# Kernel optimization log

Measured on AMD Instinct MI355X. Metric: run time of the kernel, lower is better.

The kernel has to match this reference:

```python
import jax, jax.numpy as jnp
import numpy as np

B, N, H, FD = 2, 512, 128, 5
NT, SD, L = 3, 4, 3
COPY = 10.0
EPS = 1e-6


def setup_inputs() -> dict:
    key = jax.random.key(0)
    ks = jax.random.split(key, 20)
    node_type = jax.random.randint(ks[0], (B, N, 1), 0, NT).astype(jnp.float32)
    node_state = jax.random.normal(ks[1], (B, N, SD), jnp.float32)
    node_feats = jnp.concatenate([node_type, node_state], axis=-1)  # [B,N,5]
    adj = jax.random.bernoulli(ks[2], 0.05, (B, N, N)).astype(jnp.float32)
    adj = jnp.maximum(adj, adj.transpose(0, 2, 1)) * (1.0 - jnp.eye(N, dtype=jnp.float32))
    scope_node_mask = jax.random.bernoulli(ks[3], 0.5, (B, N)).astype(jnp.float32)
    scope_edge_mask = jax.random.bernoulli(ks[4], 0.5, (B, N, N)).astype(jnp.float32)
    s = 0.02
    p = dict(
        node_feats=node_feats, adj=adj,
        scope_node_mask=scope_node_mask, scope_edge_mask=scope_edge_mask,
        W_in=jax.random.normal(ks[5], (FD, H)) * s, b_in=jnp.zeros((H,)),
        W_mp=jax.random.normal(ks[6], (L, 2 * H, H)) * s, b_mp=jnp.zeros((L, H)),
        Wt1=jax.random.normal(ks[7], (H, H)) * s, bt1=jnp.zeros((H,)),
        Wt2=jax.random.normal(ks[8], (H, NT)) * s, bt2=jnp.zeros((NT,)),
        Ws1=jax.random.normal(ks[9], (H, H)) * s, bs1=jnp.zeros((H,)),
        Ws2=jax.random.normal(ks[10], (H, SD)) * s, bs2=jnp.zeros((SD,)),
        We1=jax.random.normal(ks[11], (4 * H, H)) * s, be1=jnp.zeros((H,)),
        We2=jax.random.normal(ks[12], (H, 3)) * s, be2=jnp.zeros((3,)),
    )
    return p


def _decode_edge_logits(adj, edl, eye):
    probs = jax.nn.softmax(edl, axis=-1)
    p_keep = probs[..., 0]  # EDGE_DELTA_KEEP = 0
    p_add = probs[..., 1]   # EDGE_DELTA_ADD = 1
    cur = (adj > 0.5).astype(edl.dtype)
    p_next = jnp.clip(p_add + p_keep * cur, EPS, 1.0 - EPS)
    el = jnp.log(p_next) - jnp.log1p(-p_next)  # logit
    return jnp.where(eye[None], -1e9, el)


def _forward(node_feats, adj, scope_node_mask, scope_edge_mask,
             W_in, b_in, W_mp, b_mp, Wt1, bt1, Wt2, bt2,
             Ws1, bs1, Ws2, bs2, We1, be1, We2, be2):
    # encoder: input proj + L rounds of [h, adj@h] -> Linear -> ReLU
    h = jax.nn.relu(node_feats @ W_in + b_in)  # [B,N,H]
    for l in range(L):
        msg = jnp.einsum('bij,bjh->bih', adj, h)
        h = jax.nn.relu(jnp.concatenate([h, msg], axis=-1) @ W_mp[l] + b_mp[l])
    # node heads (2-layer MLPs)
    type_local = jax.nn.relu(h @ Wt1 + bt1) @ Wt2 + bt2      # [B,N,NT]
    state_local = jax.nn.relu(h @ Ws1 + bs1) @ Ws2 + bs2     # [B,N,SD]
    # pairwise edge-delta head
    h_i = h[:, :, None, :]
    h_j = h[:, None, :, :]
    pair = jnp.concatenate([
        jnp.broadcast_to(h_i, (B, N, N, H)),
        jnp.broadcast_to(h_j, (B, N, N, H)),
        jnp.abs(h_i - h_j),
        h_i * h_j,
    ], axis=-1)  # [B,N,N,4H]
    edl = jax.nn.relu(pair @ We1 + be1) @ We2 + be2  # [B,N,N,3]
    edl = 0.5 * (edl + edl.transpose(0, 2, 1, 3))
    eye = jnp.eye(N, dtype=bool)
    edl = jnp.where(eye[None, :, :, None], 0.0, edl)
    # merges with copy paths
    cur_type = jnp.clip(node_feats[..., 0].astype(jnp.int32), 0, NT - 1)
    copy_type = jnp.where(jnp.arange(NT) == cur_type[..., None], COPY, -COPY)
    type_full = jnp.where(scope_node_mask[..., None] != 0, type_local, copy_type)
    scope = scope_node_mask[..., None]
    state_full = scope * state_local + (1.0 - scope) * node_feats[..., 1:]
    copy_edl = jnp.broadcast_to(jnp.where(jnp.arange(3) == 0, COPY, -COPY), (B, N, N, 3))
    copy_edl = jnp.where(eye[None, :, :, None], 0.0, copy_edl)
    edl_full = jnp.where(scope_edge_mask[..., None] != 0, edl, copy_edl)
    el_full = _decode_edge_logits(adj, edl_full, eye)
    return type_full, state_full, edl_full, el_full


def reference(node_feats, adj, scope_node_mask, scope_edge_mask,
              W_in, b_in, W_mp, b_mp, Wt1, bt1, Wt2, bt2,
              Ws1, bs1, Ws2, bs2, We1, be1, We2, be2):
    return _forward(node_feats, adj, scope_node_mask, scope_edge_mask,
                    W_in, b_in, W_mp, b_mp, Wt1, bt1, Wt2, bt2,
                    Ws1, bs1, Ws2, bs2, We1, be1, We2, be2)
```

## Files before the change

### kernel.cpp

```cpp
#include <hip/hip_runtime.h>
#include <hip/hip_fp16.h>
#include <math.h>

#define B_ 2
#define N_ 512
#define H_ 128
#define NT_ 3
#define SD_ 4
#define FD_ 5

typedef float f32x4 __attribute__((ext_vector_type(4)));
typedef unsigned int u32x4 __attribute__((ext_vector_type(4)));

#define MFMA4(a0, a1, a2, a3, av, b0, b1, b2, b3) \
    asm("s_nop 1\n\t" \
        "v_mfma_f32_16x16x32_f16 %0, %4, %5, %0\n\t" \
        "v_mfma_f32_16x16x32_f16 %1, %4, %6, %1\n\t" \
        "v_mfma_f32_16x16x32_f16 %2, %4, %7, %2\n\t" \
        "v_mfma_f32_16x16x32_f16 %3, %4, %8, %3" \
        : "+v"(a0), "+v"(a1), "+v"(a2), "+v"(a3) \
        : "v"(av), "v"(b0), "v"(b1), "v"(b2), "v"(b3))

#define MFMA16F(acc, a, b) \
    asm("s_nop 1\n\tv_mfma_f32_16x16x32_f16 %0, %1, %2, %0" \
        : "+v"(acc) : "v"(a), "v"(b))

#define PKMUL(d, a, b) \
    asm("v_pk_mul_f16 %0, %1, %2" : "=v"(d) : "v"(a), "v"(b))
#define PKSUB(d, a, b) \
    asm("v_pk_add_f16 %0, %1, %2 neg_lo:[0,1] neg_hi:[0,1]" \
        : "=v"(d) : "v"(a), "v"(b))
#define CVTPKF16(d, a, b) \
    asm("v_cvt_pkrtz_f16_f32 %0, %1, %2" : "=v"(d) : "v"(a), "v"(b))

static __device__ inline unsigned short f2h(float f) {
    return __half_as_ushort(__float2half(f));
}

__global__ __launch_bounds__(128) void k_input(const float* __restrict__ feats,
                                               const float* __restrict__ W_in,
                                               const float* __restrict__ b_in,
                                               float* __restrict__ hout,
                                               const float* __restrict__ We1,
                                               const float* __restrict__ We2,
                                               unsigned short* __restrict__ wfrag,
                                               unsigned short* __restrict__ wfrag2) {
    int blk = blockIdx.x, tid = threadIdx.x;
    if (blk < B_ * N_) {
        const float* f = feats + (size_t)blk * FD_;
        float acc = b_in[tid];
#pragma unroll
        for (int k = 0; k < FD_; ++k) acc += f[k] * W_in[k * H_ + tid];
        hout[(size_t)blk * H_ + tid] = fmaxf(acc, 0.f);
        return;
    }
    if (blk < B_ * N_ + 32) {
        int t = (blk - B_ * N_) * 128 + tid;
        int lane = t & 63, cg = (t >> 6) & 7, kb = t >> 9;
        int lr = lane & 15, g = lane >> 4;
        int c = cg * 16 + lr;
        unsigned o[4];
#pragma unroll
        for (int p = 0; p < 4; ++p) {
            float a = We1[(size_t)(256 + kb * 32 + 8 * g + 2 * p) * H_ + c];
            float bq = We1[(size_t)(256 + kb * 32 + 8 * g + 2 * p + 1) * H_ + c];
            o[p] = (unsigned)f2h(a) | ((unsigned)f2h(bq) << 16);
        }
        u32x4 v = {o[0], o[1], o[2], o[3]};
        *(u32x4*)(wfrag + (size_t)t * 8) = v;
        return;
    }
    {
        int t = (blk - (B_ * N_ + 32)) * 128 + tid;
        if (t < 256) {
            int kb = t >> 6, lane = t & 63;
            int oc = lane & 15, g = lane >> 4;
            unsigned w[4];
#pragma unroll
            for (int p = 0; p < 4; ++p) {
                int k0 = kb * 32 + g * 8 + 2 * p;
                int k1 = k0 + 1;
                int c0 = ((k0 >> 6) << 6) | ((k0 & 3) << 4) | ((k0 & 63) >> 2);
                int c1 = ((k1 >> 6) << 6) | ((k1 & 3) << 4) | ((k1 & 63) >> 2);
                float v0 = (oc < 3) ? We2[c0 * 3 + oc] : 0.f;
                float v1 = (oc < 3) ? We2[c1 * 3 + oc] : 0.f;
                w[p] = (unsigned)f2h(v0) | ((unsigned)f2h(v1) << 16);
            }
            u32x4 v = {w[0], w[1], w[2], w[3]};
            *(u32x4*)(wfrag2 + (size_t)t * 8) = v;
        }
    }
}

__global__ __launch_bounds__(256) void k_mp(const float* __restrict__ hin,
                                            float* __restrict__ hout,
                                            const float* __restrict__ adj,
                                            const float* __restrict__ Wl,
                                            const float* __restrict__ bl) {
    __shared__ float xbuf[256];
    __shared__ unsigned short idxs[512];
    __shared__ float avals[512];
    __shared__ float red[256];
    __shared__ int cnt[4];
    int node = blockIdx.x;
    int b = node >> 9;
    int tid = threadIdx.x;
    int w = tid >> 6, lane = tid & 63;
    if (tid < 128) xbuf[tid] = hin[(size_t)node * H_ + tid];
    const float* arow = adj + (size_t)node * N_;
    float2 av = ((const float2*)arow)[tid];
    int cum = 0;
#pragma unroll
    for (int q2 = 0; q2 < 2; ++q2) {
        float a = (&av.x)[q2];
        bool pred = (a != 0.f);
        unsigned long long mask = __ballot(pred);
        if (pred) {
            int pos = 128 * w + cum +
                      (int)__popcll(mask & ((1ull << lane) - 1ull));
            idxs[pos] = (unsigned short)(2 * tid + q2);
            avals[pos] = a;
        }
        cum += (int)__popcll(mask);
    }
    if (lane == 0) cnt[w] = cum;
    __syncthreads();

    int c = tid & 127, q = tid >> 7;
    const float* hb = hin + ((size_t)b * N_) * H_;
    float m = 0.f;
#pragma unroll
    for (int s = 0; s < 4; ++s) {
        int ns = cnt[s];
        for (int t = q; t < ns; t += 2)
            m += avals[128 * s + t] * hb[(size_t)idxs[128 * s + t] * H_ + c];
    }
    red[q * 128 + c] = m;
    __syncthreads();
    if (q == 0) xbuf[128 + c] = red[c] + red[128 + c];
    __syncthreads();

    float acc = 0.f;
#pragma unroll 4
    for (int k = 128 * q; k < 128 * q + 128; ++k)
        acc += xbuf[k] * Wl[(size_t)k * H_ + c];
    red[q * 128 + c] = acc;
    __syncthreads();
    if (q == 0)
        hout[(size_t)node * H_ + c] =
            fmaxf(red[c] + red[128 + c] + bl[c], 0.f);
}

__global__ __launch_bounds__(128) void k_heads(
    const float* __restrict__ h, const float* __restrict__ feats,
    const float* __restrict__ snm,
    const float* __restrict__ Wt1, const float* __restrict__ bt1,
    const float* __restrict__ Wt2, const float* __restrict__ bt2,
    const float* __restrict__ Ws1, const float* __restrict__ bs1,
    const float* __restrict__ Ws2, const float* __restrict__ bs2,
    const float* __restrict__ We1, const float* __restrict__ be1,
    float* __restrict__ Acoef, float* __restrict__ Bcoef,
    unsigned short* __restrict__ hf16,
    float* __restrict__ type_out, float* __restrict__ state_out) {
    __shared__ float hi[H_], hT[H_], hS[H_];
    int node = blockIdx.x, tid = threadIdx.x;
    float hv0 = h[(size_t)node * H_ + tid];
    hi[tid] = hv0;
    hf16[(size_t)node * H_ + tid] = f2h(hv0);
    __syncthreads();
    float at = bt1[tid], as = bs1[tid], aa = be1[tid], ab = 0.f;
#pragma unroll 4
    for (int k = 0; k < H_; ++k) {
        float hv = hi[k];
        at += hv * Wt1[k * H_ + tid];
        as += hv * Ws1[k * H_ + tid];
        aa += hv * We1[k * H_ + tid];
        ab += hv * We1[(k + H_) * H_ + tid];
    }
    hT[tid] = fmaxf(at, 0.f);
    hS[tid] = fmaxf(as, 0.f);
    int c = tid;
    int kp = ((c >> 6) << 6) | ((c & 15) << 2) | ((c >> 4) & 3);
    Acoef[(size_t)node * H_ + kp] = aa;
    Bcoef[(size_t)node * H_ + kp] = ab;
    __syncthreads();
    float sm = snm[node];
    if (tid < NT_) {
        float tl = bt2[tid];
        for (int cc = 0; cc < H_; ++cc) tl += hT[cc] * Wt2[cc * NT_ + tid];
        int ct = (int)feats[(size_t)node * FD_];
        ct = ct < 0 ? 0 : (ct > NT_ - 1 ? NT_ - 1 : ct);
        float cv = (tid == ct) ? 10.f : -10.f;
        type_out[(size_t)node * NT_ + tid] = (sm != 0.f) ? tl : cv;
    }
    if (tid >= 64 && tid < 64 + SD_) {
        int s = tid - 64;
        float sl = bs2[s];
        for (int cc = 0; cc < H_; ++cc) sl += hS[cc] * Ws2[cc * SD_ + s];
        state_out[(size_t)node * SD_ + s] =
            sm * sl + (1.f - sm) * feats[(size_t)node * FD_ + 1 + s];
    }
}

__global__ __launch_bounds__(256, 2) void k_pair2(
    const unsigned short* __restrict__ hf16,
    const float* __restrict__ Acp, const float* __restrict__ Bcp,
    const unsigned short* __restrict__ wfrag,
    const unsigned short* __restrict__ wfrag2,
    const float* __restrict__ be2,
    float* __restrict__ edl_out) {

    __shared__ unsigned short tile[2][64][128];
    __shared__ float sbuf[2][64][3];

    int bid = blockIdx.x;
    int b = 0, r = bid;
    if (r >= 1280) { b = 1; r -= 1280; }
    int jtile, i;
    if (r < 128)      { jtile = 0; i = r; }
    else if (r < 384) { jtile = 1; i = r - 128; }
    else if (r < 768) { jtile = 2; i = r - 384; }
    else              { jtile = 3; i = r - 768; }
    int JT0 = jtile << 7;
    int bN = b << 9;

    int tid = threadIdx.x;
    int wave = tid >> 6, lane = tid & 63;
    int jh = wave >> 1, ch = wave & 1;
    int lr = lane & 15, g = lane >> 4;

    u32x4 Bf[4][8];
#pragma unroll
    for (int ct = 0; ct < 4; ++ct)
#pragma unroll
        for (int kb = 0; kb < 8; ++kb)
            Bf[ct][kb] = *(const u32x4*)(wfrag +
                (((size_t)kb * 8 + (ch * 4 + ct)) * 64 + lane) * 8);

    u32x4 Bf2[4];
#pragma unroll
    for (int kb = 0; kb < 4; ++kb)
        Bf2[kb] = *(const u32x4*)(wfrag2 + ((size_t)kb * 64 + lane) * 8);

    const unsigned short* hirow = hf16 + (size_t)(bN + i) * H_;
    u32x4 him[4];
#pragma unroll
    for (int m = 0; m < 4; ++m)
        him[m] = *(const u32x4*)(hirow + 32 * m + 8 * g);

    f32x4 AcoI = *(const f32x4*)(Acp + (size_t)(bN + i) * H_ + ch * 64 + lr * 4);
    f32x4 BcoI = *(const f32x4*)(Bcp + (size_t)(bN + i) * H_ + ch * 64 + lr * 4);

    char* tb0 = (char*)&tile[0][0][0];
    char* tb1 = (char*)&tile[1][0][0];

    for (int jhalf = 0; jhalf < 2; ++jhalf) {
        int J0 = JT0 + jhalf * 64;
#pragma unroll
        for (int jt = 0; jt < 2; ++jt) {
            int jloc0 = jh * 32 + jt * 16;
            const unsigned short* hjp =
                hf16 + (size_t)(bN + J0 + jloc0 + lr) * H_ + 8 * g;
            u32x4 hjall[4];
#pragma unroll
            for (int m = 0; m < 4; ++m)
                hjall[m] = *(const u32x4*)(hjp + 32 * m);
            f32x4 BcJv[4], AcJv[4];
#pragma unroll
            for (int rr = 0; rr < 4; ++rr) {
                size_t jn = (size_t)(bN + J0 + jloc0 + 4 * g + rr) * H_ +
                            ch * 64 + lr * 4;
                BcJv[rr] = *(const f32x4*)(Bcp + jn);
                AcJv[rr] = *(const f32x4*)(Acp + jn);
            }

            f32x4 acc0 = {0.f,0.f,0.f,0.f}, acc1 = {0.f,0.f,0.f,0.f};
            f32x4 acc2 = {0.f,0.f,0.f,0.f}, acc3 = {0.f,0.f,0.f,0.f};

#pragma unroll
            for (int m = 0; m < 4; ++m) {
                u32x4 tav, uav;
#pragma unroll
                for (int p = 0; p < 4; ++p) {
                    unsigned hip_ = him[m][p], hjp_ = hjall[m][p];
                    unsigned u_, d_;
                    PKMUL(u_, hip_, hjp_);
                    PKSUB(d_, hip_, hjp_);
                    uav[p] = u_;
                    tav[p] = d_ & 0x7fff7fffu;
                }
                MFMA4(acc0, acc1, acc2, acc3, tav,
                      Bf[0][m], Bf[1][m], Bf[2][m], Bf[3][m]);
                MFMA4(acc0, acc1, acc2, acc3, uav,
                      Bf[0][4 + m], Bf[1][4 + m], Bf[2][4 + m], Bf[3][4 + m]);
            }
            asm("s_nop 7\n\ts_nop 7\n\ts_nop 3"
                : "+v"(acc0), "+v"(acc1), "+v"(acc2), "+v"(acc3));

#pragma unroll
            for (int rr = 0; rr < 4; ++rr) {
                int jloc = jloc0 + 4 * g + rr;
                float h10 = fmaxf(acc0[rr] + AcoI[0] + BcJv[rr][0], 0.f);
                float h11 = fmaxf(acc1[rr] + AcoI[1] + BcJv[rr][1], 0.f);
                float h12 = fmaxf(acc2[rr] + AcoI[2] + BcJv[rr][2], 0.f);
                float h13 = fmaxf(acc3[rr] + AcoI[3] + BcJv[rr][3], 0.f);
                float h20 = fmaxf(acc0[rr] + AcJv[rr][0] + BcoI[0], 0.f);
                float h21 = fmaxf(acc1[rr] + AcJv[rr][1] + BcoI[1], 0.f);
                float h22 = fmaxf(acc2[rr] + AcJv[rr][2] + BcoI[2], 0.f);
                float h23 = fmaxf(acc3[rr] + AcJv[rr][3] + BcoI[3], 0.f);
                unsigned w10, w11, w20, w21;
                CVTPKF16(w10, h10, h11); CVTPKF16(w11, h12, h13);
                CVTPKF16(w20, h20, h21); CVTPKF16(w21, h22, h23);
                int byte = jloc * 256 + ch * 128 + lr * 8;
                byte ^= (jloc & 7) << 4;
                uint2 v1; v1.x = w10; v1.y = w11;
                uint2 v2; v2.x = w20; v2.y = w21;
                *(uint2*)(tb0 + byte) = v1;
                *(uint2*)(tb1 + byte) = v2;
            }
        }
        __syncthreads();

        f32x4 pacc0 = {0.f,0.f,0.f,0.f}, pacc1 = {0.f,0.f,0.f,0.f};
#pragma unroll
        for (int p = 0; p < 2; ++p) {
            int f = wave + 4 * p;
            int orient = f >> 2, sub = f & 3;
            char* tb = orient ? tb1 : tb0;
            int jloc = sub * 16 + lr;
#pragma unroll
            for (int kb = 0; kb < 4; ++kb) {
                int byte = jloc * 256 + kb * 64 + g * 16;
                byte ^= (jloc & 7) << 4;
                u32x4 a = *(const u32x4*)(tb + byte);
                if (p == 0) { MFMA16F(pacc0, a, Bf2[kb]); }
                else        { MFMA16F(pacc1, a, Bf2[kb]); }
            }
        }
        asm("s_nop 7\n\ts_nop 7\n\ts_nop 3" : "+v"(pacc0), "+v"(pacc1));

        if (lr < 3) {
#pragma unroll
            for (int p = 0; p < 2; ++p) {
                int f = wave + 4 * p;
                int orient = f >> 2, sub = f & 3;
                f32x4 pa = p ? pacc1 : pacc0;
#pragma unroll
                for (int rr = 0; rr < 4; ++rr) {
                    int jloc = sub * 16 + 4 * g + rr;
                    sbuf[orient][jloc][lr] = pa[rr];
                }
            }
        }
        __syncthreads();

        if (tid < 192) {
            int jloc = tid / 3, comp = tid - jloc * 3;
            float v = 0.5f * (sbuf[0][jloc][comp] + sbuf[1][jloc][comp]) +
                      be2[comp];
            edl_out[((size_t)(bN + i) * N_ + (J0 + jloc)) * 3 + comp] = v;
        }
    }
}

__global__ __launch_bounds__(256) void k_tr(float* __restrict__ edl,
                                            float* __restrict__ el,
                                            const float* __restrict__ sem,
                                            const float* __restrict__ adj) {
    __shared__ float ss[3][16][17];
    int tid = threadIdx.x;
    int r = tid >> 4, c = tid & 15;
    int bid = blockIdx.x;
    int b = 0, t = bid;
    if (t >= 528) { b = 1; t -= 528; }
    int J = (int)((sqrtf(8.f * (float)t + 1.f) - 1.f) * 0.5f);
    while ((J + 1) * (J + 2) / 2 <= t) ++J;
    while (J * (J + 1) / 2 > t) --J;
    int I = t - J * (J + 1) / 2;
    int i0 = I * 16, j0 = J * 16;
    int bN = b << 9;

    {
        const float* src = edl + ((size_t)(bN + i0 + r) * N_ + (j0 + c)) * 3;
        ss[0][r][c] = src[0];
        ss[1][r][c] = src[1];
        ss[2][r][c] = src[2];
    }
    __syncthreads();

    for (int pass = 0; pass < 2; ++pass) {
        if (pass == 1 && I == J) break;
        int gi, gj;
        float s0, s1, s2;
        if (I == J) {
            gi = i0 + r; gj = j0 + c;
            int lo = r <= c ? r : c, hi = r <= c ? c : r;
            s0 = ss[0][lo][hi]; s1 = ss[1][lo][hi]; s2 = ss[2][lo][hi];
        } else if (pass == 0) {
            gi = i0 + r; gj = j0 + c;
            s0 = ss[0][r][c]; s1 = ss[1][r][c]; s2 = ss[2][r][c];
        } else {
            gi = j0 + r; gj = i0 + c;
            s0 = ss[0][c][r]; s1 = ss[1][c][r]; s2 = ss[2][c][r];
        }
        size_t p = (size_t)(bN + gi) * N_ + gj;
        if (gi == gj) {
            edl[p * 3 + 0] = 0.f; edl[p * 3 + 1] = 0.f; edl[p * 3 + 2] = 0.f;
            el[p] = -1e9f;
        } else {
            float msk = sem[p];
            float e0 = (msk != 0.f) ? s0 : 10.f;
            float e1 = (msk != 0.f) ? s1 : -10.f;
            float e2 = (msk != 0.f) ? s2 : -10.f;
            edl[p * 3 + 0] = e0; edl[p * 3 + 1] = e1; edl[p * 3 + 2] = e2;
            float a = adj[p];
            float cur = (a > 0.5f) ? 1.f : 0.f;
            float mx = fmaxf(e0, fmaxf(e1, e2));
            float x0 = expf(e0 - mx), x1 = expf(e1 - mx), x2 = expf(e2 - mx);
            float inv = 1.f / (x0 + x1 + x2);
            float pn = x1 * inv + x0 * inv * cur;
            pn = fminf(fmaxf(pn, 1e-6f), 1.f - 1e-6f);
            el[p] = logf(pn) - log1pf(-pn);
        }
    }
}

extern "C" void kernel_launch(void* const* d_in, const int* in_sizes, int n_in,
                              void* d_out, int out_size, void* d_ws,
                              size_t ws_size, hipStream_t stream) {
    const float* feats = (const float*)d_in[0];
    const float* adj   = (const float*)d_in[1];
    const float* snm   = (const float*)d_in[2];
    const float* sem   = (const float*)d_in[3];
    const float* W_in  = (const float*)d_in[4];
    const float* b_in  = (const float*)d_in[5];
    const float* W_mp  = (const float*)d_in[6];
    const float* b_mp  = (const float*)d_in[7];
    const float* Wt1 = (const float*)d_in[8],  *bt1 = (const float*)d_in[9];
    const float* Wt2 = (const float*)d_in[10], *bt2 = (const float*)d_in[11];
    const float* Ws1 = (const float*)d_in[12], *bs1 = (const float*)d_in[13];
    const float* Ws2 = (const float*)d_in[14], *bs2 = (const float*)d_in[15];
    const float* We1 = (const float*)d_in[16], *be1 = (const float*)d_in[17];
    const float* We2 = (const float*)d_in[18], *be2 = (const float*)d_in[19];

    float* out = (float*)d_out;
    float* type_out  = out;
    float* state_out = out + 3072;
    float* edl_out   = out + 7168;
    float* el_out    = out + 7168 + 1572864;

    float* ws = (float*)d_ws;
    float* hA = ws;
    float* hB = ws + 131072;
    float* Bcp = ws + 262144;
    unsigned short* hf16   = (unsigned short*)(ws + 393216);
    unsigned short* wfrag  = (unsigned short*)(ws + 458752);
    unsigned short* wfrag2 = (unsigned short*)(ws + 475136);
    float* Acp = hA;

    k_input<<<B_ * N_ + 34, 128, 0, stream>>>(feats, W_in, b_in, hA,
                                              We1, We2, wfrag, wfrag2);
    k_mp<<<B_ * N_, 256, 0, stream>>>(hA, hB, adj,
                                      W_mp + 0 * 2 * H_ * H_, b_mp + 0 * H_);
    k_mp<<<B_ * N_, 256, 0, stream>>>(hB, hA, adj,
                                      W_mp + 1 * 2 * H_ * H_, b_mp + 1 * H_);
    k_mp<<<B_ * N_, 256, 0, stream>>>(hA, hB, adj,
                                      W_mp + 2 * 2 * H_ * H_, b_mp + 2 * H_);
    k_heads<<<B_ * N_, H_, 0, stream>>>(hB, feats, snm, Wt1, bt1, Wt2, bt2,
                                        Ws1, bs1, Ws2, bs2, We1, be1,
                                        Acp, Bcp, hf16, type_out, state_out);
    k_pair2<<<2560, 256, 0, stream>>>(hf16, Acp, Bcp, wfrag, wfrag2,
                                      be2, edl_out);
    k_tr<<<1056, 256, 0, stream>>>(edl_out, el_out, sem, adj);
}
```

Baseline: 131.4 us.

## Split pair kernel channel work across 8 waves instead of 4

Raises k_pair2 from 4 to 8 waves per block. Each wave now owns 2 of the 8 output column tiles instead of 4, so it issues 2 MFMAs per k-step and holds half as many weight fragments in registers. The Acoef/Bcoef permutation and the We2 fragment layout are changed to the new 2-wide channel interleave, and the second-stage projection gives one 16-row sub-tile to each wave. The aim is more parallelism and latency hiding per block by cutting per-wave register pressure, at the cost of more waves sharing LDS and barriers, and a higher thread count per block that can constrain occupancy.

```diff
diff --git a/kernel.cpp b/kernel.cpp
--- a/kernel.cpp
+++ b/kernel.cpp
@@ -12,14 +12,11 @@
 typedef float f32x4 __attribute__((ext_vector_type(4)));
 typedef unsigned int u32x4 __attribute__((ext_vector_type(4)));
 
-#define MFMA4(a0, a1, a2, a3, av, b0, b1, b2, b3) \
+#define MFMA2(a0, a1, av, b0, b1) \
     asm("s_nop 1\n\t" \
-        "v_mfma_f32_16x16x32_f16 %0, %4, %5, %0\n\t" \
-        "v_mfma_f32_16x16x32_f16 %1, %4, %6, %1\n\t" \
-        "v_mfma_f32_16x16x32_f16 %2, %4, %7, %2\n\t" \
-        "v_mfma_f32_16x16x32_f16 %3, %4, %8, %3" \
-        : "+v"(a0), "+v"(a1), "+v"(a2), "+v"(a3) \
-        : "v"(av), "v"(b0), "v"(b1), "v"(b2), "v"(b3))
+        "v_mfma_f32_16x16x32_f16 %0, %2, %3, %0\n\t" \
+        "v_mfma_f32_16x16x32_f16 %1, %2, %4, %1" \
+        : "+v"(a0), "+v"(a1) : "v"(av), "v"(b0), "v"(b1))
 
 #define MFMA16F(acc, a, b) \
     asm("s_nop 1\n\tv_mfma_f32_16x16x32_f16 %0, %1, %2, %0" \
@@ -80,8 +77,8 @@
             for (int p = 0; p < 4; ++p) {
                 int k0 = kb * 32 + g * 8 + 2 * p;
                 int k1 = k0 + 1;
-                int c0 = ((k0 >> 6) << 6) | ((k0 & 3) << 4) | ((k0 & 63) >> 2);
-                int c1 = ((k1 >> 6) << 6) | ((k1 & 3) << 4) | ((k1 & 63) >> 2);
+                int c0 = ((k0 >> 5) << 5) | ((k0 & 1) << 4) | ((k0 & 31) >> 1);
+                int c1 = ((k1 >> 5) << 5) | ((k1 & 1) << 4) | ((k1 & 31) >> 1);
                 float v0 = (oc < 3) ? We2[c0 * 3 + oc] : 0.f;
                 float v1 = (oc < 3) ? We2[c1 * 3 + oc] : 0.f;
                 w[p] = (unsigned)f2h(v0) | ((unsigned)f2h(v1) << 16);
@@ -180,7 +177,7 @@
     hT[tid] = fmaxf(at, 0.f);
     hS[tid] = fmaxf(as, 0.f);
     int c = tid;
-    int kp = ((c >> 6) << 6) | ((c & 15) << 2) | ((c >> 4) & 3);
+    int kp = ((c >> 5) << 5) | ((c & 15) << 1) | ((c >> 4) & 1);
     Acoef[(size_t)node * H_ + kp] = aa;
     Bcoef[(size_t)node * H_ + kp] = ab;
     __syncthreads();
@@ -202,7 +199,7 @@
     }
 }
 
-__global__ __launch_bounds__(256, 2) void k_pair2(
+__global__ __launch_bounds__(512, 2) void k_pair2(
     const unsigned short* __restrict__ hf16,
     const float* __restrict__ Acp, const float* __restrict__ Bcp,
     const unsigned short* __restrict__ wfrag,
@@ -226,16 +223,16 @@
 
     int tid = threadIdx.x;
     int wave = tid >> 6, lane = tid & 63;
-    int jh = wave >> 1, ch = wave & 1;
+    int jh = wave >> 2, ch = wave & 3;
     int lr = lane & 15, g = lane >> 4;
 
-    u32x4 Bf[4][8];
-#pragma unroll
-    for (int ct = 0; ct < 4; ++ct)
+    u32x4 Bf[2][8];
+#pragma unroll
+    for (int ct = 0; ct < 2; ++ct)
 #pragma unroll
         for (int kb = 0; kb < 8; ++kb)
             Bf[ct][kb] = *(const u32x4*)(wfrag +
-                (((size_t)kb * 8 + (ch * 4 + ct)) * 64 + lane) * 8);
+                (((size_t)kb * 8 + (ch * 2 + ct)) * 64 + lane) * 8);
 
     u32x4 Bf2[4];
 #pragma unroll
@@ -248,8 +245,8 @@
     for (int m = 0; m < 4; ++m)
         him[m] = *(const u32x4*)(hirow + 32 * m + 8 * g);
 
-    f32x4 AcoI = *(const f32x4*)(Acp + (size_t)(bN + i) * H_ + ch * 64 + lr * 4);
-    f32x4 BcoI = *(const f32x4*)(Bcp + (size_t)(bN + i) * H_ + ch * 64 + lr * 4);
+    float2 AcoI = *(const float2*)(Acp + (size_t)(bN + i) * H_ + ch * 32 + lr * 2);
+    float2 BcoI = *(const float2*)(Bcp + (size_t)(bN + i) * H_ + ch * 32 + lr * 2);
 
     char* tb0 = (char*)&tile[0][0][0];
     char* tb1 = (char*)&tile[1][0][0];
@@ -265,17 +262,16 @@
 #pragma unroll
             for (int m = 0; m < 4; ++m)
                 hjall[m] = *(const u32x4*)(hjp + 32 * m);
-            f32x4 BcJv[4], AcJv[4];
+            float2 BcJv[4], AcJv[4];
 #pragma unroll
             for (int rr = 0; rr < 4; ++rr) {
                 size_t jn = (size_t)(bN + J0 + jloc0 + 4 * g + rr) * H_ +
-                            ch * 64 + lr * 4;
-                BcJv[rr] = *(const f32x4*)(Bcp + jn);
-                AcJv[rr] = *(const f32x4*)(Acp + jn);
+                            ch * 32 + lr * 2;
+                BcJv[rr] = *(const float2*)(Bcp + jn);
+                AcJv[rr] = *(const float2*)(Acp + jn);
             }
 
             f32x4 acc0 = {0.f,0.f,0.f,0.f}, acc1 = {0.f,0.f,0.f,0.f};
-            f32x4 acc2 = {0.f,0.f,0.f,0.f}, acc3 = {0.f,0.f,0.f,0.f};
 
 #pragma unroll
             for (int m = 0; m < 4; ++m) {
@@ -289,67 +285,46 @@
                     uav[p] = u_;
                     tav[p] = d_ & 0x7fff7fffu;
                 }
-                MFMA4(acc0, acc1, acc2, acc3, tav,
-                      Bf[0][m], Bf[1][m], Bf[2][m], Bf[3][m]);
-                MFMA4(acc0, acc1, acc2, acc3, uav,
-                      Bf[0][4 + m], Bf[1][4 + m], Bf[2][4 + m], Bf[3][4 + m]);
-            }
-            asm("s_nop 7\n\ts_nop 7\n\ts_nop 3"
-                : "+v"(acc0), "+v"(acc1), "+v"(acc2), "+v"(acc3));
+                MFMA2(acc0, acc1, tav, Bf[0][m], Bf[1][m]);
+                MFMA2(acc0, acc1, uav, Bf[0][4 + m], Bf[1][4 + m]);
+            }
+            asm("s_nop 7\n\ts_nop 7\n\ts_nop 3" : "+v"(acc0), "+v"(acc1));
 
 #pragma unroll
             for (int rr = 0; rr < 4; ++rr) {
                 int jloc = jloc0 + 4 * g + rr;
-                float h10 = fmaxf(acc0[rr] + AcoI[0] + BcJv[rr][0], 0.f);
-                float h11 = fmaxf(acc1[rr] + AcoI[1] + BcJv[rr][1], 0.f);
-                float h12 = fmaxf(acc2[rr] + AcoI[2] + BcJv[rr][2], 0.f);
-                float h13 = fmaxf(acc3[rr] + AcoI[3] + BcJv[rr][3], 0.f);
-                float h20 = fmaxf(acc0[rr] + AcJv[rr][0] + BcoI[0], 0.f);
-                float h21 = fmaxf(acc1[rr] + AcJv[rr][1] + BcoI[1], 0.f);
-                float h22 = fmaxf(acc2[rr] + AcJv[rr][2] + BcoI[2], 0.f);
-                float h23 = fmaxf(acc3[rr] + AcJv[rr][3] + BcoI[3], 0.f);
-                unsigned w10, w11, w20, w21;
-                CVTPKF16(w10, h10, h11); CVTPKF16(w11, h12, h13);
-                CVTPKF16(w20, h20, h21); CVTPKF16(w21, h22, h23);
-                int byte = jloc * 256 + ch * 128 + lr * 8;
+                float h10 = fmaxf(acc0[rr] + AcoI.x + BcJv[rr].x, 0.f);
+                float h11 = fmaxf(acc1[rr] + AcoI.y + BcJv[rr].y, 0.f);
+                float h20 = fmaxf(acc0[rr] + AcJv[rr].x + BcoI.x, 0.f);
+                float h21 = fmaxf(acc1[rr] + AcJv[rr].y + BcoI.y, 0.f);
+                unsigned w1, w2;
+                CVTPKF16(w1, h10, h11);
+                CVTPKF16(w2, h20, h21);
+                int byte = jloc * 256 + ch * 64 + lr * 4;
                 byte ^= (jloc & 7) << 4;
-                uint2 v1; v1.x = w10; v1.y = w11;
-                uint2 v2; v2.x = w20; v2.y = w21;
-                *(uint2*)(tb0 + byte) = v1;
-                *(uint2*)(tb1 + byte) = v2;
+                *(unsigned*)(tb0 + byte) = w1;
+                *(unsigned*)(tb1 + byte) = w2;
             }
         }
         __syncthreads();
 
-        f32x4 pacc0 = {0.f,0.f,0.f,0.f}, pacc1 = {0.f,0.f,0.f,0.f};
-#pragma unroll
-        for (int p = 0; p < 2; ++p) {
-            int f = wave + 4 * p;
-            int orient = f >> 2, sub = f & 3;
+        {
+            int orient = wave >> 2, sub = wave & 3;
             char* tb = orient ? tb1 : tb0;
             int jloc = sub * 16 + lr;
+            f32x4 pacc = {0.f, 0.f, 0.f, 0.f};
 #pragma unroll
             for (int kb = 0; kb < 4; ++kb) {
                 int byte = jloc * 256 + kb * 64 + g * 16;
                 byte ^= (jloc & 7) << 4;
                 u32x4 a = *(const u32x4*)(tb + byte);
-                if (p == 0) { MFMA16F(pacc0, a, Bf2[kb]); }
-                else        { MFMA16F(pacc1, a, Bf2[kb]); }
-            }
-        }
-        asm("s_nop 7\n\ts_nop 7\n\ts_nop 3" : "+v"(pacc0), "+v"(pacc1));
-
-        if (lr < 3) {
-#pragma unroll
-            for (int p = 0; p < 2; ++p) {
-                int f = wave + 4 * p;
-                int orient = f >> 2, sub = f & 3;
-                f32x4 pa = p ? pacc1 : pacc0;
-#pragma unroll
-                for (int rr = 0; rr < 4; ++rr) {
-                    int jloc = sub * 16 + 4 * g + rr;
-                    sbuf[orient][jloc][lr] = pa[rr];
-                }
+                MFMA16F(pacc, a, Bf2[kb]);
+            }
+            asm("s_nop 7\n\ts_nop 7\n\ts_nop 3" : "+v"(pacc));
+            if (lr < 3) {
+#pragma unroll
+                for (int rr = 0; rr < 4; ++rr)
+                    sbuf[orient][sub * 16 + 4 * g + rr][lr] = pacc[rr];
             }
         }
         __syncthreads();
@@ -469,7 +444,7 @@
     k_heads<<<B_ * N_, H_, 0, stream>>>(hB, feats, snm, Wt1, bt1, Wt2, bt2,
                                         Ws1, bs1, Ws2, bs2, We1, be1,
                                         Acp, Bcp, hf16, type_out, state_out);
-    k_pair2<<<2560, 256, 0, stream>>>(hf16, Acp, Bcp, wfrag, wfrag2,
+    k_pair2<<<2560, 512, 0, stream>>>(hf16, Acp, Bcp, wfrag, wfrag2,
                                       be2, edl_out);
     k_tr<<<1056, 256, 0, stream>>>(edl_out, el_out, sem, adj);
 }
```

Measured after the change: 166.1 us. 1.26x slower.
